# Optimization experiments

Measured on AMD Instinct MI355X. Metric: run time of the kernel, lower is better.

## Reference

```python
import jax, jax.numpy as jnp
import numpy as np

B, S, E = 2, 2048, 1024
H, W_SIZE = 16, 128
D = E // H


def setup_inputs() -> dict:
    key = jax.random.key(0)
    ks = jax.random.split(key, 7)
    std = 1.0 / np.sqrt(E)
    return {
        "x": jax.random.normal(ks[0], (B, S, E), dtype=jnp.float32),
        "Wq": jax.random.normal(ks[1], (E, E), dtype=jnp.float32) * std,
        "bq": jax.random.normal(ks[2], (E,), dtype=jnp.float32) * std,
        "Wk": jax.random.normal(ks[3], (E, E), dtype=jnp.float32) * std,
        "bk": jax.random.normal(ks[4], (E,), dtype=jnp.float32) * std,
        "Wv": jax.random.normal(ks[5], (E, E), dtype=jnp.float32) * std,
        "bv": jax.random.normal(ks[6], (E,), dtype=jnp.float32) * std,
    }


def reference(x, Wq, bq, Wk, bk, Wv, bv):
    b, s, e = x.shape
    scale = jnp.float32(D) ** -0.5
    # torch Linear: y = x @ W.T + b
    # Faithful to original: view() splits [b, s, e] -> [b, H, s, D] WITHOUT transpose
    q = (x @ Wq.T + bq).reshape(b, H, s, D)
    k = (x @ Wk.T + bk).reshape(b, H, s, D)
    v = (x @ Wv.T + bv).reshape(b, H, s, D)
    # window: scores kept for j in [max(0, i - w), min(s, i + w)), zeros elsewhere
    i = jnp.arange(s)[:, None]
    j = jnp.arange(s)[None, :]
    mask = (j >= i - W_SIZE) & (j < i + W_SIZE)  # [s, s]
    qk = jnp.einsum("bhid,bhjd->bhij", q, k)
    # out-of-window entries are ZERO (not -inf) and softmax is over the full row,
    # exactly matching the original zero-padded score tensor.
    scores = jnp.where(mask, qk, 0.0) * scale
    probs = jax.nn.softmax(scores, axis=-1)
    out = jnp.einsum("bhij,bhjd->bhid", probs, v)  # [b, H, s, D]
    out = out.transpose(0, 2, 1, 3).reshape(b, s, e)
    return out
```

## Files before the change

kernel.cpp:

```cpp
#include <hip/hip_runtime.h>
#include <math.h>

#define S_LEN 2048
#define E_DIM 1024
#define NHEAD 16
#define HD 64
#define WIN 128
#define NB 2
#define MTOT (NB * S_LEN)
#define NMAT 3072

typedef float f32x4 __attribute__((ext_vector_type(4)));
typedef short bf16x8 __attribute__((ext_vector_type(8)));

#define GLOAD_LDS(g, l) __builtin_amdgcn_global_load_lds( \
    (const __attribute__((address_space(1))) unsigned int*)(g), \
    (__attribute__((address_space(3))) unsigned int*)(l), 16, 0, 0)

__device__ __forceinline__ unsigned short f2bf(float f) {
    unsigned u = __float_as_uint(f);
    u += 0x7fffu + ((u >> 16) & 1u);
    return (unsigned short)(u >> 16);
}
__device__ __forceinline__ float bf2f(unsigned short u) {
    return __uint_as_float(((unsigned)u) << 16);
}

__global__ __launch_bounds__(256) void convert_kernel(
    const float* __restrict__ x, const float* __restrict__ wq,
    const float* __restrict__ wk, const float* __restrict__ wv,
    unsigned short* __restrict__ xb, unsigned short* __restrict__ wb)
{
    const int NXQ = MTOT * E_DIM / 4;
    const int NWQ = E_DIM * E_DIM / 4;
    const int TOT = NXQ + 3 * NWQ;
    for (int i = blockIdx.x * 256 + threadIdx.x; i < TOT; i += gridDim.x * 256) {
        const float* src; unsigned short* dst; int off;
        if (i < NXQ)               { src = x;  dst = xb;                     off = i; }
        else if (i < NXQ + NWQ)    { src = wq; dst = wb;                     off = i - NXQ; }
        else if (i < NXQ + 2*NWQ)  { src = wk; dst = wb + E_DIM * E_DIM;     off = i - NXQ - NWQ; }
        else                       { src = wv; dst = wb + 2 * E_DIM * E_DIM; off = i - NXQ - 2*NWQ; }
        float4 v = ((const float4*)src)[off];
        ushort4 o;
        o.x = f2bf(v.x); o.y = f2bf(v.y); o.z = f2bf(v.z); o.w = f2bf(v.w);
        ((ushort4*)dst)[off] = o;
    }
}

__global__ __launch_bounds__(256) void gemm_mfma(
    const unsigned short* __restrict__ Ab, const unsigned short* __restrict__ Bb,
    const float* __restrict__ bq, const float* __restrict__ bk, const float* __restrict__ bv,
    unsigned short* __restrict__ Qb, unsigned short* __restrict__ Kb,
    unsigned short* __restrict__ Vb)
{
    __shared__ __align__(256) unsigned short As[128 * 64];
    __shared__ __align__(256) unsigned short Bs[128 * 64];
    const int tid  = threadIdx.x;
    const int lane = tid & 63;
    const int w    = tid >> 6;
    const int wm   = w & 1, wn = w >> 1;
    const int m0   = blockIdx.y * 128;
    const int n0   = blockIdx.x * 128;
    const int l15  = lane & 15, l4 = lane >> 4;

    f32x4 acc[16] = {};

    for (int k0 = 0; k0 < E_DIM; k0 += 64) {
        #pragma unroll
        for (int is = 0; is < 4; ++is) {
            int gid = is * 256 + tid;
            int r = gid >> 3, sl = gid & 7;
            int gran = sl ^ (r & 7);
            int wbs = is * 256 + (tid & 192);
            GLOAD_LDS(Ab + (size_t)(m0 + r) * E_DIM + k0 + gran * 8, As + wbs * 8);
            GLOAD_LDS(Bb + (size_t)(n0 + r) * E_DIM + k0 + gran * 8, Bs + wbs * 8);
        }
        __syncthreads();
        #pragma unroll
        for (int kk = 0; kk < 2; ++kk) {
            bf16x8 af[4], bfr[4];
            int sa = (kk * 4 + l4) ^ (l15 & 7);
            #pragma unroll
            for (int t = 0; t < 4; ++t) {
                int ra = wm * 64 + t * 16 + l15;
                af[t]  = *(const bf16x8*)&As[ra * 64 + sa * 8];
                int rb = wn * 64 + t * 16 + l15;
                bfr[t] = *(const bf16x8*)&Bs[rb * 64 + sa * 8];
            }
            #pragma unroll
            for (int mt = 0; mt < 4; ++mt)
                #pragma unroll
                for (int nt = 0; nt < 4; ++nt)
                    acc[mt * 4 + nt] = __builtin_amdgcn_mfma_f32_16x16x32_bf16(
                        af[mt], bfr[nt], acc[mt * 4 + nt], 0, 0, 0);
        }
        __syncthreads();
    }

    const int sel = n0 >> 10;
    const float* bias = (sel == 0) ? bq : ((sel == 1) ? bk : bv);
    unsigned short* Yb = (sel == 0) ? Qb : ((sel == 1) ? Kb : Vb);
    const int nbase = (n0 & 1023) + wn * 64;
    #pragma unroll
    for (int mt = 0; mt < 4; ++mt) {
        #pragma unroll
        for (int nt = 0; nt < 4; ++nt) {
            int n = nbase + nt * 16 + l15;
            int c = n >> 6, d = n & 63;
            float bb = bias[n];
            #pragma unroll
            for (int r = 0; r < 4; ++r) {
                int m = m0 + wm * 64 + mt * 16 + l4 * 4 + r;
                int b = m >> 11, s = m & 2047;
                int h = s >> 7;
                int i = ((s & 127) << 4) + c;
                Yb[(((size_t)(b * 16 + h) * S_LEN + i) << 6) + d] =
                    f2bf(acc[mt * 4 + nt][r] + bb);
            }
        }
    }
}

__global__ __launch_bounds__(256) void transpose_vtot(
    const unsigned short* __restrict__ Vb, unsigned short* __restrict__ VTb,
    float* __restrict__ vt)
{
    __shared__ unsigned short t[64][72];
    const int bh = blockIdx.y;
    const int it0 = blockIdx.x * 64;
    const int tid = threadIdx.x;
    const unsigned short* src = Vb + ((size_t)bh * S_LEN + it0) * HD;
    {
        int r = tid >> 2, c0 = (tid & 3) * 16;
        #pragma unroll
        for (int k = 0; k < 4; ++k) {
            ushort4 a = *(const ushort4*)&src[r * 64 + c0 + k * 4];
            *(ushort4*)&t[r][c0 + k * 4] = a;
        }
    }
    __syncthreads();
    {
        int d = tid >> 2, seg = (tid & 3) * 16;
        unsigned short v[16];
        float s = 0.f;
        #pragma unroll
        for (int k = 0; k < 16; ++k) { v[k] = t[seg + k][d]; s += bf2f(v[k]); }
        unsigned short* dst = VTb + ((size_t)bh * HD + d) * S_LEN + it0 + seg;
        #pragma unroll
        for (int k = 0; k < 4; ++k)
            *(ushort4*)&dst[k * 4] = *(const ushort4*)&v[k * 4];
        s += __shfl_xor(s, 1);
        s += __shfl_xor(s, 2);
        if ((tid & 3) == 0) atomicAdd(&vt[bh * HD + d], s);
    }
}

__global__ __launch_bounds__(256) void attn_mfma(
    const unsigned short* __restrict__ Qb, const unsigned short* __restrict__ Kb,
    const unsigned short* __restrict__ VTb, const float* __restrict__ vtot,
    float* __restrict__ out)
{
    __shared__ __align__(256) unsigned short qs[128 * 64];
    __shared__ __align__(256) unsigned short ks[2][64 * 64];
    __shared__ __align__(256) unsigned short vts[2][64 * 64];
    __shared__ __align__(16)  unsigned short ps[4][32 * 72];

    const int qt = blockIdx.x, bh = blockIdx.y;
    const int b = bh >> 4, h = bh & 15;
    const int i0 = qt * 128;
    const int tid = threadIdx.x;
    const int w = tid >> 6, lane = tid & 63;
    const int l15 = lane & 15, quad = lane >> 4;

    const unsigned short* Qp = Qb + (size_t)bh * S_LEN * HD;
    const unsigned short* Kp = Kb + (size_t)bh * S_LEN * HD;
    const unsigned short* Vp = VTb + (size_t)bh * HD * S_LEN;

    #pragma unroll
    for (int it = 0; it < 4; ++it) {
        int gid = it * 256 + tid;
        int r = gid >> 3, sl = gid & 7;
        int gran = sl ^ (r & 7);
        int wbs = it * 256 + (tid & 192);
        GLOAD_LDS(Qp + (size_t)(i0 + r) * HD + gran * 8, qs + wbs * 8);
    }

    const int j_begin = (i0 - WIN > 0) ? i0 - WIN : 0;
    const int j_end   = (i0 + 256 < S_LEN) ? i0 + 256 : S_LEN;
    const int n_ch    = (j_end - j_begin) >> 6;

    #pragma unroll
    for (int it = 0; it < 2; ++it) {
        int gid = it * 256 + tid;
        int r = gid >> 3, sl = gid & 7;
        int gran = sl ^ (r & 7);
        int wbs = it * 256 + (tid & 192);
        GLOAD_LDS(Kp + (size_t)(j_begin + r) * HD + gran * 8, ks[0] + wbs * 8);
        GLOAD_LDS(Vp + (size_t)r * S_LEN + j_begin + gran * 8, vts[0] + wbs * 8);
    }
    __syncthreads();

    bf16x8 aq[2][2];
    #pragma unroll
    for (int q2 = 0; q2 < 2; ++q2) {
        int row = w * 32 + q2 * 16 + l15;
        aq[q2][0] = *(const bf16x8*)&qs[(row * 8 + (quad ^ (row & 7))) * 8];
        aq[q2][1] = *(const bf16x8*)&qs[(row * 8 + ((4 + quad) ^ (row & 7))) * 8];
    }
    bf16x8 bones;
    #pragma unroll
    for (int t = 0; t < 8; ++t) bones[t] = (short)0x3F80;

    f32x4 acc_o[2][4] = {};
    f32x4 acc_sum[2] = {};
    unsigned short* psw = &ps[w][0];

    for (int c = 0; c < n_ch; ++c) {
        const int cb = c & 1;
        const int jc0 = j_begin + c * 64;

        if (c + 1 < n_ch) {
            const int jn0 = jc0 + 64;
            #pragma unroll
            for (int it = 0; it < 2; ++it) {
                int gid = it * 256 + tid;
                int r = gid >> 3, sl = gid & 7;
                int gran = sl ^ (r & 7);
                int wbs = it * 256 + (tid & 192);
                GLOAD_LDS(Kp + (size_t)(jn0 + r) * HD + gran * 8, ks[1 - cb] + wbs * 8);
                GLOAD_LDS(Vp + (size_t)r * S_LEN + jn0 + gran * 8, vts[1 - cb] + wbs * 8);
            }
        }

        f32x4 sacc[2][4] = {};
        const unsigned short* kb = ks[cb];
        #pragma unroll
        for (int kk = 0; kk < 2; ++kk) {
            #pragma unroll
            for (int jt = 0; jt < 4; ++jt) {
                int row = jt * 16 + l15;
                bf16x8 bk = *(const bf16x8*)&kb[(row * 8 + ((kk * 4 + quad) ^ (row & 7))) * 8];
                sacc[0][jt] = __builtin_amdgcn_mfma_f32_16x16x32_bf16(aq[0][kk], bk, sacc[0][jt], 0, 0, 0);
                sacc[1][jt] = __builtin_amdgcn_mfma_f32_16x16x32_bf16(aq[1][kk], bk, sacc[1][jt], 0, 0, 0);
            }
        }

        #pragma unroll
        for (int q2 = 0; q2 < 2; ++q2) {
            #pragma unroll
            for (int jt = 0; jt < 4; ++jt) {
                int jg = jc0 + jt * 16 + l15;
                #pragma unroll
                for (int reg = 0; reg < 4; ++reg) {
                    int i = i0 + w * 32 + q2 * 16 + quad * 4 + reg;
                    bool valid = (jg >= i - WIN) && (jg < i + WIN);
                    float p = valid ? __expf(sacc[q2][jt][reg] * 0.125f) - 1.f : 0.f;
                    psw[(q2 * 16 + quad * 4 + reg) * 72 + jt * 16 + l15] = f2bf(p);
                }
            }
        }
        bf16x8 ap[2][2];
        #pragma unroll
        for (int q2 = 0; q2 < 2; ++q2) {
            ap[q2][0] = *(const bf16x8*)&psw[(q2 * 16 + l15) * 72 + quad * 8];
            ap[q2][1] = *(const bf16x8*)&psw[(q2 * 16 + l15) * 72 + 32 + quad * 8];
        }

        const unsigned short* vb = vts[cb];
        #pragma unroll
        for (int kst = 0; kst < 2; ++kst) {
            #pragma unroll
            for (int dt = 0; dt < 4; ++dt) {
                int row = dt * 16 + l15;
                bf16x8 bv_ = *(const bf16x8*)&vb[(row * 8 + ((kst * 4 + quad) ^ (row & 7))) * 8];
                acc_o[0][dt] = __builtin_amdgcn_mfma_f32_16x16x32_bf16(ap[0][kst], bv_, acc_o[0][dt], 0, 0, 0);
                acc_o[1][dt] = __builtin_amdgcn_mfma_f32_16x16x32_bf16(ap[1][kst], bv_, acc_o[1][dt], 0, 0, 0);
            }
            acc_sum[0] = __builtin_amdgcn_mfma_f32_16x16x32_bf16(ap[0][kst], bones, acc_sum[0], 0, 0, 0);
            acc_sum[1] = __builtin_amdgcn_mfma_f32_16x16x32_bf16(ap[1][kst], bones, acc_sum[1], 0, 0, 0);
        }
        __syncthreads();
    }

    const float* vtp = vtot + bh * HD;
    float vtv[4];
    #pragma unroll
    for (int dt = 0; dt < 4; ++dt) vtv[dt] = vtp[dt * 16 + l15];
    #pragma unroll
    for (int q2 = 0; q2 < 2; ++q2) {
        #pragma unroll
        for (int reg = 0; reg < 4; ++reg) {
            int i = i0 + w * 32 + q2 * 16 + quad * 4 + reg;
            float inv = 1.f / (acc_sum[q2][reg] + (float)S_LEN);
            float* op = out + (((size_t)(b * S_LEN + i)) * NHEAD + h) * HD;
            #pragma unroll
            for (int dt = 0; dt < 4; ++dt)
                op[dt * 16 + l15] = (acc_o[q2][dt][reg] + vtv[dt]) * inv;
        }
    }
}

extern "C" void kernel_launch(void* const* d_in, const int* in_sizes, int n_in,
                              void* d_out, int out_size, void* d_ws, size_t ws_size,
                              hipStream_t stream)
{
    const float* x  = (const float*)d_in[0];
    const float* Wq = (const float*)d_in[1];
    const float* bq = (const float*)d_in[2];
    const float* Wk = (const float*)d_in[3];
    const float* bk = (const float*)d_in[4];
    const float* Wv = (const float*)d_in[5];
    const float* bv = (const float*)d_in[6];
    float* out = (float*)d_out;

    const size_t NY = (size_t)MTOT * E_DIM;
    unsigned short* xb  = (unsigned short*)d_ws;
    unsigned short* wb  = xb + NY;
    unsigned short* Qb  = wb + (size_t)3 * E_DIM * E_DIM;
    unsigned short* Kb  = Qb + NY;
    unsigned short* Vb  = Kb + NY;
    float* vt = (float*)(Vb + NY);
    unsigned short* VTb = xb;

    convert_kernel<<<1792, 256, 0, stream>>>(x, Wq, Wk, Wv, xb, wb);
    gemm_mfma<<<dim3(NMAT / 128, MTOT / 128), 256, 0, stream>>>(xb, wb, bq, bk, bv, Qb, Kb, Vb);
    hipMemsetAsync(vt, 0, (size_t)NB * NHEAD * HD * sizeof(float), stream);
    transpose_vtot<<<dim3(S_LEN / 64, NB * NHEAD), 256, 0, stream>>>(Vb, VTb, vt);
    attn_mfma<<<dim3(S_LEN / 128, NB * NHEAD), 256, 0, stream>>>(Qb, Kb, VTb, vt, out);
}
```

Baseline: 152.6 us.

## Fuse V column sums into GEMM epilogue and transpose V in attention LDS

Removes the separate transpose_vtot kernel. The V column totals are now reduced from the GEMM accumulators (plus 128×bias) and added with atomics in the GEMM epilogue. The V transpose is done per chunk inside the attention kernel through an LDS scratch buffer. The P buffer now shares space with the Q tile to save LDS. This trades one kernel launch and one global round trip of V for an extra LDS transpose and an extra __syncthreads per chunk. V prefetch also loses its double buffering.

```diff
diff --git a/kernel.cpp b/kernel.cpp
--- a/kernel.cpp
+++ b/kernel.cpp
@@ -51,7 +51,7 @@
     const unsigned short* __restrict__ Ab, const unsigned short* __restrict__ Bb,
     const float* __restrict__ bq, const float* __restrict__ bk, const float* __restrict__ bv,
     unsigned short* __restrict__ Qb, unsigned short* __restrict__ Kb,
-    unsigned short* __restrict__ Vb)
+    unsigned short* __restrict__ Vb, float* __restrict__ vt)
 {
     __shared__ __align__(256) unsigned short As[128 * 64];
     __shared__ __align__(256) unsigned short Bs[128 * 64];
@@ -119,51 +119,36 @@
             }
         }
     }
-}
-
-__global__ __launch_bounds__(256) void transpose_vtot(
-    const unsigned short* __restrict__ Vb, unsigned short* __restrict__ VTb,
-    float* __restrict__ vt)
-{
-    __shared__ unsigned short t[64][72];
-    const int bh = blockIdx.y;
-    const int it0 = blockIdx.x * 64;
-    const int tid = threadIdx.x;
-    const unsigned short* src = Vb + ((size_t)bh * S_LEN + it0) * HD;
-    {
-        int r = tid >> 2, c0 = (tid & 3) * 16;
-        #pragma unroll
-        for (int k = 0; k < 4; ++k) {
-            ushort4 a = *(const ushort4*)&src[r * 64 + c0 + k * 4];
-            *(ushort4*)&t[r][c0 + k * 4] = a;
-        }
-    }
-    __syncthreads();
-    {
-        int d = tid >> 2, seg = (tid & 3) * 16;
-        unsigned short v[16];
-        float s = 0.f;
-        #pragma unroll
-        for (int k = 0; k < 16; ++k) { v[k] = t[seg + k][d]; s += bf2f(v[k]); }
-        unsigned short* dst = VTb + ((size_t)bh * HD + d) * S_LEN + it0 + seg;
-        #pragma unroll
-        for (int k = 0; k < 4; ++k)
-            *(ushort4*)&dst[k * 4] = *(const ushort4*)&v[k * 4];
-        s += __shfl_xor(s, 1);
-        s += __shfl_xor(s, 2);
-        if ((tid & 3) == 0) atomicAdd(&vt[bh * HD + d], s);
+
+    if (sel == 2) {
+        const int bh = (m0 >> 11) * 16 + ((m0 & 2047) >> 7);
+        #pragma unroll
+        for (int nt = 0; nt < 4; ++nt) {
+            float s = 0.f;
+            #pragma unroll
+            for (int mt = 0; mt < 4; ++mt)
+                #pragma unroll
+                for (int r = 0; r < 4; ++r) s += acc[mt * 4 + nt][r];
+            s += __shfl_xor(s, 16);
+            s += __shfl_xor(s, 32);
+            if (l4 == 0) {
+                int n = nbase + nt * 16 + l15;
+                float add = s + ((wm == 0) ? 128.f * bias[n] : 0.f);
+                atomicAdd(&vt[bh * HD + (n & 63)], add);
+            }
+        }
     }
 }
 
 __global__ __launch_bounds__(256) void attn_mfma(
     const unsigned short* __restrict__ Qb, const unsigned short* __restrict__ Kb,
-    const unsigned short* __restrict__ VTb, const float* __restrict__ vtot,
+    const unsigned short* __restrict__ Vb, const float* __restrict__ vtot,
     float* __restrict__ out)
 {
-    __shared__ __align__(256) unsigned short qs[128 * 64];
+    __shared__ __align__(256) unsigned short qps[9216];
     __shared__ __align__(256) unsigned short ks[2][64 * 64];
-    __shared__ __align__(256) unsigned short vts[2][64 * 64];
-    __shared__ __align__(16)  unsigned short ps[4][32 * 72];
+    __shared__ __align__(256) unsigned short vts[64 * 64];
+    __shared__ __align__(256) unsigned short vscr[64 * 64];
 
     const int qt = blockIdx.x, bh = blockIdx.y;
     const int b = bh >> 4, h = bh & 15;
@@ -174,7 +159,7 @@
 
     const unsigned short* Qp = Qb + (size_t)bh * S_LEN * HD;
     const unsigned short* Kp = Kb + (size_t)bh * S_LEN * HD;
-    const unsigned short* Vp = VTb + (size_t)bh * HD * S_LEN;
+    const unsigned short* Vp = Vb + (size_t)bh * S_LEN * HD;
 
     #pragma unroll
     for (int it = 0; it < 4; ++it) {
@@ -182,7 +167,7 @@
         int r = gid >> 3, sl = gid & 7;
         int gran = sl ^ (r & 7);
         int wbs = it * 256 + (tid & 192);
-        GLOAD_LDS(Qp + (size_t)(i0 + r) * HD + gran * 8, qs + wbs * 8);
+        GLOAD_LDS(Qp + (size_t)(i0 + r) * HD + gran * 8, qps + wbs * 8);
     }
 
     const int j_begin = (i0 - WIN > 0) ? i0 - WIN : 0;
@@ -196,7 +181,7 @@
         int gran = sl ^ (r & 7);
         int wbs = it * 256 + (tid & 192);
         GLOAD_LDS(Kp + (size_t)(j_begin + r) * HD + gran * 8, ks[0] + wbs * 8);
-        GLOAD_LDS(Vp + (size_t)r * S_LEN + j_begin + gran * 8, vts[0] + wbs * 8);
+        GLOAD_LDS(Vp + (size_t)(j_begin + r) * HD + gran * 8, vscr + wbs * 8);
     }
     __syncthreads();
 
@@ -204,8 +189,8 @@
     #pragma unroll
     for (int q2 = 0; q2 < 2; ++q2) {
         int row = w * 32 + q2 * 16 + l15;
-        aq[q2][0] = *(const bf16x8*)&qs[(row * 8 + (quad ^ (row & 7))) * 8];
-        aq[q2][1] = *(const bf16x8*)&qs[(row * 8 + ((4 + quad) ^ (row & 7))) * 8];
+        aq[q2][0] = *(const bf16x8*)&qps[(row * 8 + (quad ^ (row & 7))) * 8];
+        aq[q2][1] = *(const bf16x8*)&qps[(row * 8 + ((4 + quad) ^ (row & 7))) * 8];
     }
     bf16x8 bones;
     #pragma unroll
@@ -213,11 +198,25 @@
 
     f32x4 acc_o[2][4] = {};
     f32x4 acc_sum[2] = {};
-    unsigned short* psw = &ps[w][0];
+    unsigned short* psw = qps + w * 2304;
+
+    const int td = tid & 63;
+    const int toct = tid >> 6;
 
     for (int c = 0; c < n_ch; ++c) {
         const int cb = c & 1;
         const int jc0 = j_begin + c * 64;
+
+        #pragma unroll
+        for (int pc = 0; pc < 2; ++pc) {
+            int oct = toct + pc * 4;
+            bf16x8 vv;
+            #pragma unroll
+            for (int t = 0; t < 8; ++t)
+                vv[t] = (short)vscr[(oct * 8 + t) * 64 + (((td >> 3) ^ t) * 8) + (td & 7)];
+            *(bf16x8*)&vts[td * 64 + ((oct ^ (td & 7)) * 8)] = vv;
+        }
+        __syncthreads();
 
         if (c + 1 < n_ch) {
             const int jn0 = jc0 + 64;
@@ -228,7 +227,7 @@
                 int gran = sl ^ (r & 7);
                 int wbs = it * 256 + (tid & 192);
                 GLOAD_LDS(Kp + (size_t)(jn0 + r) * HD + gran * 8, ks[1 - cb] + wbs * 8);
-                GLOAD_LDS(Vp + (size_t)r * S_LEN + jn0 + gran * 8, vts[1 - cb] + wbs * 8);
+                GLOAD_LDS(Vp + (size_t)(jn0 + r) * HD + gran * 8, vscr + wbs * 8);
             }
         }
 
@@ -266,13 +265,12 @@
             ap[q2][1] = *(const bf16x8*)&psw[(q2 * 16 + l15) * 72 + 32 + quad * 8];
         }
 
-        const unsigned short* vb = vts[cb];
         #pragma unroll
         for (int kst = 0; kst < 2; ++kst) {
             #pragma unroll
             for (int dt = 0; dt < 4; ++dt) {
                 int row = dt * 16 + l15;
-                bf16x8 bv_ = *(const bf16x8*)&vb[(row * 8 + ((kst * 4 + quad) ^ (row & 7))) * 8];
+                bf16x8 bv_ = *(const bf16x8*)&vts[(row * 8 + ((kst * 4 + quad) ^ (row & 7))) * 8];
                 acc_o[0][dt] = __builtin_amdgcn_mfma_f32_16x16x32_bf16(ap[0][kst], bv_, acc_o[0][dt], 0, 0, 0);
                 acc_o[1][dt] = __builtin_amdgcn_mfma_f32_16x16x32_bf16(ap[1][kst], bv_, acc_o[1][dt], 0, 0, 0);
             }
@@ -320,11 +318,9 @@
     unsigned short* Kb  = Qb + NY;
     unsigned short* Vb  = Kb + NY;
     float* vt = (float*)(Vb + NY);
-    unsigned short* VTb = xb;
 
     convert_kernel<<<1792, 256, 0, stream>>>(x, Wq, Wk, Wv, xb, wb);
-    gemm_mfma<<<dim3(NMAT / 128, MTOT / 128), 256, 0, stream>>>(xb, wb, bq, bk, bv, Qb, Kb, Vb);
     hipMemsetAsync(vt, 0, (size_t)NB * NHEAD * HD * sizeof(float), stream);
-    transpose_vtot<<<dim3(S_LEN / 64, NB * NHEAD), 256, 0, stream>>>(Vb, VTb, vt);
-    attn_mfma<<<dim3(S_LEN / 128, NB * NHEAD), 256, 0, stream>>>(Qb, Kb, VTb, vt, out);
-}
+    gemm_mfma<<<dim3(NMAT / 128, MTOT / 128), 256, 0, stream>>>(xb, wb, bq, bk, bv, Qb, Kb, Vb, vt);
+    attn_mfma<<<dim3(S_LEN / 128, NB * NHEAD), 256, 0, stream>>>(Qb, Kb, Vb, vt, out);
+}
```

Measured after the change: 151.4 us. About the same (-0.8%).
